# Kernel optimization log

Hardware: AMD Instinct MI355X
Metric: run time of the kernel (lower is better)

The kernel has to match this reference:

```python
import jax, jax.numpy as jnp
import numpy as np

D_MODEL = 1024
N_HEADS = 16
D_K = D_MODEL // N_HEADS
SCALE = 1.0 / np.sqrt(D_K).astype(np.float32)
NEG = -1000000000.0


def setup_inputs() -> dict:
    key = jax.random.key(0)
    ks = jax.random.split(key, 5)
    B, S = 2, 2048
    query = jax.random.normal(ks[0], (B, S, D_MODEL), dtype=jnp.float32)
    k_in = jax.random.normal(ks[1], (B, S, D_MODEL), dtype=jnp.float32)
    v_in = jax.random.normal(ks[2], (B, S, D_MODEL), dtype=jnp.float32)
    # causal mask, broadcast over batch and heads; 0 entries get -1e9
    mask = jnp.tril(jnp.ones((S, S), dtype=jnp.int32))[None, None, :, :]
    w_qkv = jax.random.normal(ks[3], (D_MODEL, 3 * D_MODEL), dtype=jnp.float32) * (1.0 / np.sqrt(D_MODEL))
    w_o = jax.random.normal(ks[4], (D_MODEL, D_MODEL), dtype=jnp.float32) * (1.0 / np.sqrt(D_MODEL))
    return {"query": query, "key": k_in, "value": v_in, "mask": mask, "w_qkv": w_qkv, "w_o": w_o}


def reference(query, key, value, mask, w_qkv, w_o):
    # NOTE: original module ignores `key`/`value`; q,k,v all come from `query`.
    B, S, _ = query.shape
    qkv = query @ w_qkv                       # [B,S,3D]
    q, k, v = jnp.split(qkv, 3, axis=-1)
    def heads(x):
        return x.reshape(B, S, N_HEADS, D_K).transpose(0, 2, 1, 3)  # [B,H,S,dk]
    Q, K, V = heads(q), heads(k), heads(v)
    scores = jnp.einsum('bhqd,bhkd->bhqk', Q, K) * SCALE            # [B,H,S,S]
    scores = jnp.where(mask == 0, NEG, scores)
    attn = jax.nn.softmax(scores, axis=-1)
    # Dropout(0.1) treated as eval-mode identity for a deterministic reference.
    context = jnp.einsum('bhqk,bhkd->bhqd', attn, V)                # [B,H,S,dk]
    context = context.transpose(0, 2, 1, 3).reshape(B, S, D_MODEL)
    return context @ w_o
```

## Files before the change

kernel.cpp:

```cpp
#include <hip/hip_runtime.h>
#include <stdint.h>
#include <type_traits>


typedef __attribute__((ext_vector_type(8))) short bf16x8;
typedef __attribute__((ext_vector_type(4))) float f32x4;

#define LOG2E 1.44269504088896340736f
#define QSCALE (0.125f * LOG2E)

__device__ __forceinline__ unsigned short f2b(float f) {
  union { float f; unsigned int i; } x; x.f = f;
  unsigned int i = x.i;
  return (unsigned short)((i + 0x7FFFu + ((i >> 16) & 1u)) >> 16);
}

__device__ __forceinline__ void async16(const void* g, void* l) {
  __builtin_amdgcn_global_load_lds(
      (__attribute__((address_space(1))) void*)g,
      (__attribute__((address_space(3))) void*)l, 16, 0, 0);
}

__device__ __forceinline__ f32x4 mfma16(bf16x8 a, bf16x8 b, f32x4 c) {
  return __builtin_amdgcn_mfma_f32_16x16x32_bf16(a, b, c, 0, 0, 0);
}

__global__ __launch_bounds__(256) void cvt_x(const float* __restrict__ src,
                                             unsigned short* __restrict__ dst) {
  const size_t i = ((size_t)blockIdx.x * 256 + threadIdx.x) * 8;
  float4 a = *(const float4*)(src + i);
  float4 b = *(const float4*)(src + i + 4);
  unsigned short e[8];
  e[0] = f2b(a.x); e[1] = f2b(a.y); e[2] = f2b(a.z); e[3] = f2b(a.w);
  e[4] = f2b(b.x); e[5] = f2b(b.y); e[6] = f2b(b.z); e[7] = f2b(b.w);
  *(uint4*)(dst + i) = *(const uint4*)e;
}

__global__ __launch_bounds__(256) void transpose_cvt(
    const float* __restrict__ src, unsigned short* __restrict__ dst, int R,
    int Ccols, int scale_cols, float scale) {
  __shared__ __align__(16) unsigned short Lt[64 * 64];
  const int r0 = blockIdx.x * 64, c0 = blockIdx.y * 64;
  const float s = (c0 < scale_cols) ? scale : 1.0f;
  const int t = threadIdx.x;
#pragma unroll
  for (int it = 0; it < 4; ++it) {
    int c = it * 256 + t;
    int sr = c >> 4, co = (c & 15) * 4;
    float4 v = *(const float4*)(src + (size_t)(r0 + sr) * Ccols + c0 + co);
    Lt[(co + 0) * 64 + sr] = f2b(v.x * s);
    Lt[(co + 1) * 64 + sr] = f2b(v.y * s);
    Lt[(co + 2) * 64 + sr] = f2b(v.z * s);
    Lt[(co + 3) * 64 + sr] = f2b(v.w * s);
  }
  __syncthreads();
#pragma unroll
  for (int it = 0; it < 2; ++it) {
    int c = it * 256 + t;
    int dr = c >> 3, so = (c & 7) * 8;
    *(uint4*)(dst + (size_t)(c0 + dr) * R + r0 + so) =
        *(const uint4*)(Lt + dr * 64 + so);
  }
}

template <typename CT>
__global__ __launch_bounds__(256) void gemm_bt(
    const unsigned short* __restrict__ A, const unsigned short* __restrict__ Bt,
    CT* __restrict__ C, int M, int N, int K) {
  __shared__ __align__(16) unsigned short As[128 * 32];
  __shared__ __align__(16) unsigned short Bs[128 * 32];
  const int t = threadIdx.x;
  const int w = t >> 6, l = t & 63;
  const int m0 = blockIdx.y * 128, n0 = blockIdx.x * 128;
  const int wm = (w >> 1) * 64, wn = (w & 1) * 64;
  const int lrow = l & 15, lk = (l >> 4) * 8;

  f32x4 acc[4][4] = {};

  for (int k0 = 0; k0 < K; k0 += 32) {
    __syncthreads();
#pragma unroll
    for (int r = 0; r < 2; ++r) {
      const int c = r * 256 + t;
      async16(A + (size_t)(m0 + (c >> 2)) * K + k0 + (c & 3) * 8,
              As + (size_t)(r * 256 + w * 64) * 8);
      async16(Bt + (size_t)(n0 + (c >> 2)) * K + k0 + (c & 3) * 8,
              Bs + (size_t)(r * 256 + w * 64) * 8);
    }
    asm volatile("s_waitcnt vmcnt(0)" ::: "memory");
    __syncthreads();

    bf16x8 af[4], bf[4];
#pragma unroll
    for (int i = 0; i < 4; ++i)
      af[i] = *(const bf16x8*)(As + (wm + i * 16 + lrow) * 32 + lk);
#pragma unroll
    for (int j = 0; j < 4; ++j)
      bf[j] = *(const bf16x8*)(Bs + (wn + j * 16 + lrow) * 32 + lk);
#pragma unroll
    for (int i = 0; i < 4; ++i)
#pragma unroll
      for (int j = 0; j < 4; ++j)
        acc[i][j] = mfma16(af[i], bf[j], acc[i][j]);
  }

#pragma unroll
  for (int i = 0; i < 4; ++i)
#pragma unroll
    for (int j = 0; j < 4; ++j)
#pragma unroll
      for (int r = 0; r < 4; ++r) {
        int gr = m0 + wm + i * 16 + (l >> 4) * 4 + r;
        int gc = n0 + wn + j * 16 + (l & 15);
        if constexpr (std::is_same<CT, unsigned short>::value)
          C[(size_t)gr * N + gc] = f2b(acc[i][j][r]);
        else
          C[(size_t)gr * N + gc] = acc[i][j][r];
      }
}

__global__ __launch_bounds__(256) void v_relayout(
    const unsigned short* __restrict__ qkv, unsigned short* __restrict__ Vt) {
  __shared__ __align__(16) unsigned short Lt[64 * 64];
  const int s0 = blockIdx.x * 64;
  const int bh = blockIdx.y;
  const int b = bh >> 4, h = bh & 15;
  const int t = threadIdx.x;
#pragma unroll
  for (int r = 0; r < 2; ++r) {
    int c = r * 256 + t;
    int sr = c >> 3, doff = (c & 7) * 8;
    uint4 v = *(const uint4*)(qkv + (size_t)(b * 2048 + s0 + sr) * 3072 + 2048 +
                              h * 64 + doff);
    const unsigned short* e = (const unsigned short*)&v;
#pragma unroll
    for (int j = 0; j < 8; ++j) Lt[(doff + j) * 64 + sr] = e[j];
  }
  __syncthreads();
#pragma unroll
  for (int r = 0; r < 2; ++r) {
    int c = r * 256 + t;
    int dr = c >> 3, so = (c & 7) * 8;
    *(uint4*)(Vt + ((size_t)bh * 64 + dr) * 2048 + s0 + so) =
        *(const uint4*)(Lt + dr * 64 + so);
  }
}

__global__ __launch_bounds__(256) void attn_fwd(
    const unsigned short* __restrict__ qkv,
    const unsigned short* __restrict__ Vt,
    unsigned short* __restrict__ ctx) {
  __shared__ __align__(16) unsigned short Ks[2][64 * 64];
  __shared__ __align__(16) unsigned short Vs[2][64 * 64];
  __shared__ __align__(16) unsigned short Ps[4][16 * 72];

  const int ti = blockIdx.x;
  const int bh = blockIdx.y;
  const int b = bh >> 4, h = bh & 15;
  const int t = threadIdx.x, w = t >> 6, l = t & 63;
  const int lm = l & 15, lq = l >> 4;
  const int sw = lm & 7;
  const int c0 = (lq ^ sw) * 8;
  const int c1 = ((lq + 4) ^ sw) * 8;

  const int qt0[2] = {ti * 64, (31 - ti) * 64};
  const int ktmax = 31 - ti;

  const unsigned short* Qp = qkv + (size_t)(b * 2048) * 3072 + h * 64;
  const unsigned short* Kp = qkv + (size_t)(b * 2048) * 3072 + 1024 + h * 64;
  const unsigned short* Vb = Vt + (size_t)bh * 64 * 2048;

  bf16x8 qf[2][2];
#pragma unroll
  for (int qt = 0; qt < 2; ++qt) {
    const int qrow = qt0[qt] + w * 16 + lm;
    qf[qt][0] = *(const bf16x8*)(Qp + (size_t)qrow * 3072 + lq * 8);
    qf[qt][1] = *(const bf16x8*)(Qp + (size_t)qrow * 3072 + 32 + lq * 8);
  }

  f32x4 oacc[2][4] = {};
  float lsum[2][4] = {{0.f, 0.f, 0.f, 0.f}, {0.f, 0.f, 0.f, 0.f}};

#pragma unroll
  for (int r = 0; r < 2; ++r) {
    int cl = r * 256 + t;
    int row = cl >> 3, cp = cl & 7;
    int so = ((cp ^ (row & 7)) * 8);
    async16(Kp + (size_t)row * 3072 + so,
            Ks[0] + (size_t)(r * 256 + w * 64) * 8);
    async16(Vb + (size_t)row * 2048 + so,
            Vs[0] + (size_t)(r * 256 + w * 64) * 8);
  }

  for (int kt = 0; kt <= ktmax; ++kt) {
    const int cur = kt & 1;
    asm volatile("s_waitcnt vmcnt(0)" ::: "memory");
    __syncthreads();
    if (kt < ktmax) {
      const int nk0 = (kt + 1) * 64;
#pragma unroll
      for (int r = 0; r < 2; ++r) {
        int cl = r * 256 + t;
        int row = cl >> 3, cp = cl & 7;
        int so = ((cp ^ (row & 7)) * 8);
        async16(Kp + (size_t)(nk0 + row) * 3072 + so,
                Ks[cur ^ 1] + (size_t)(r * 256 + w * 64) * 8);
        async16(Vb + (size_t)row * 2048 + nk0 + so,
                Vs[cur ^ 1] + (size_t)(r * 256 + w * 64) * 8);
      }
    }
    const unsigned short* Kc = Ks[cur];
    const unsigned short* Vc = Vs[cur];

#pragma unroll
    for (int qt = 0; qt < 2; ++qt) {
      if (qt == 0 && kt > ti) continue;
      f32x4 sacc[4] = {};
#pragma unroll
      for (int nt = 0; nt < 4; ++nt) {
        const unsigned short* kr = Kc + (nt * 16 + lm) * 64;
        bf16x8 bk0 = *(const bf16x8*)(kr + c0);
        bf16x8 bk1 = *(const bf16x8*)(kr + c1);
        sacc[nt] = mfma16(qf[qt][0], bk0, sacc[nt]);
        sacc[nt] = mfma16(qf[qt][1], bk1, sacc[nt]);
      }

      const bool diag = (kt == ((qt == 0) ? ti : ktmax));
#pragma unroll
      for (int nt = 0; nt < 4; ++nt)
#pragma unroll
        for (int r = 0; r < 4; ++r) {
          float p = exp2f(sacc[nt][r]);
          if (diag && (nt * 16 + lm) > (w * 16 + lq * 4 + r)) p = 0.f;
          lsum[qt][r] += p;
          Ps[w][(lq * 4 + r) * 72 + nt * 16 + lm] = f2b(p);
        }
      asm volatile("s_waitcnt lgkmcnt(0)" ::: "memory");

#pragma unroll
      for (int ks = 0; ks < 2; ++ks) {
        bf16x8 pa = *(const bf16x8*)(&Ps[w][lm * 72 + ks * 32 + lq * 8]);
        const int cc = (ks == 0) ? c0 : c1;
#pragma unroll
        for (int nt = 0; nt < 4; ++nt) {
          bf16x8 vb = *(const bf16x8*)(Vc + (nt * 16 + lm) * 64 + cc);
          oacc[qt][nt] = mfma16(pa, vb, oacc[qt][nt]);
        }
      }
    }
  }

#pragma unroll
  for (int qt = 0; qt < 2; ++qt) {
#pragma unroll
    for (int d = 1; d < 16; d <<= 1)
#pragma unroll
      for (int r = 0; r < 4; ++r)
        lsum[qt][r] += __shfl_xor(lsum[qt][r], d, 64);
    float rinv[4];
#pragma unroll
    for (int r = 0; r < 4; ++r) rinv[r] = 1.f / lsum[qt][r];
#pragma unroll
    for (int nt = 0; nt < 4; ++nt)
#pragma unroll
      for (int r = 0; r < 4; ++r) {
        size_t tok = (size_t)b * 2048 + qt0[qt] + w * 16 + lq * 4 + r;
        ctx[tok * 1024 + h * 64 + nt * 16 + lm] = f2b(oacc[qt][nt][r] * rinv[r]);
      }
  }
}

extern "C" void kernel_launch(void* const* d_in, const int* in_sizes, int n_in,
                              void* d_out, int out_size, void* d_ws,
                              size_t ws_size, hipStream_t stream) {
  const float* query = (const float*)d_in[0];
  const float* w_qkv = (const float*)d_in[4];
  const float* w_o = (const float*)d_in[5];
  float* out = (float*)d_out;

  unsigned short* ws = (unsigned short*)d_ws;
  unsigned short* wqkvT = ws;
  unsigned short* woT = wqkvT + (size_t)3072 * 1024;
  unsigned short* Xb = woT + (size_t)1024 * 1024;
  unsigned short* qkv = Xb + (size_t)4096 * 1024;
  unsigned short* Vt = qkv + (size_t)4096 * 3072;
  unsigned short* ctx = Xb;

  cvt_x<<<dim3(2048), 256, 0, stream>>>(query, Xb);
  transpose_cvt<<<dim3(16, 48), 256, 0, stream>>>(w_qkv, wqkvT, 1024, 3072,
                                                  1024, QSCALE);
  transpose_cvt<<<dim3(16, 16), 256, 0, stream>>>(w_o, woT, 1024, 1024, 0,
                                                  1.0f);
  gemm_bt<unsigned short><<<dim3(24, 32), 256, 0, stream>>>(Xb, wqkvT, qkv,
                                                            4096, 3072, 1024);
  v_relayout<<<dim3(32, 32), 256, 0, stream>>>(qkv, Vt);
  attn_fwd<<<dim3(16, 32), 256, 0, stream>>>(qkv, Vt, ctx);
  gemm_bt<float><<<dim3(8, 32), 256, 0, stream>>>(ctx, woT, out, 4096, 1024,
                                                  1024);
}
```

Before: 232.8 us.

## Split attention KV tiles across two warp groups and shrink output GEMM tile

Attention blocks grow to 512 threads: two groups of four warps each process alternating K/V tiles, then combine partial output accumulators and row sums through shared memory before normalising. This doubles the work in flight per block but drops the double-buffer prefetch overlap and adds a final reduction. The output projection uses a new 64x128-tile GEMM launched on twice as many blocks to fill more CUs. The P-matrix conversion to bf16 now truncates instead of rounding, which saves a few ALU ops at some accuracy cost.

```diff
diff --git a/kernel.cpp b/kernel.cpp
--- a/kernel.cpp
+++ b/kernel.cpp
@@ -13,6 +13,10 @@
   union { float f; unsigned int i; } x; x.f = f;
   unsigned int i = x.i;
   return (unsigned short)((i + 0x7FFFu + ((i >> 16) & 1u)) >> 16);
+}
+__device__ __forceinline__ unsigned short f2b_trunc(float f) {
+  union { float f; unsigned int i; } x; x.f = f;
+  return (unsigned short)(x.i >> 16);
 }
 
 __device__ __forceinline__ void async16(const void* g, void* l) {
@@ -119,6 +123,58 @@
       }
 }
 
+__global__ __launch_bounds__(256) void gemm_o(
+    const unsigned short* __restrict__ A, const unsigned short* __restrict__ Bt,
+    float* __restrict__ C, int M, int N, int K) {
+  __shared__ __align__(16) unsigned short As[64 * 32];
+  __shared__ __align__(16) unsigned short Bs[128 * 32];
+  const int t = threadIdx.x;
+  const int w = t >> 6, l = t & 63;
+  const int m0 = blockIdx.y * 64, n0 = blockIdx.x * 128;
+  const int wm = (w & 1) * 32, wn = (w >> 1) * 64;
+  const int lrow = l & 15, lk = (l >> 4) * 8;
+
+  f32x4 acc[2][4] = {};
+
+  for (int k0 = 0; k0 < K; k0 += 32) {
+    __syncthreads();
+    async16(A + (size_t)(m0 + (t >> 2)) * K + k0 + (t & 3) * 8,
+            As + (size_t)(w * 64) * 8);
+#pragma unroll
+    for (int r = 0; r < 2; ++r) {
+      const int c = r * 256 + t;
+      async16(Bt + (size_t)(n0 + (c >> 2)) * K + k0 + (c & 3) * 8,
+              Bs + (size_t)(r * 256 + w * 64) * 8);
+    }
+    asm volatile("s_waitcnt vmcnt(0)" ::: "memory");
+    __syncthreads();
+
+    bf16x8 af[2], bf[4];
+#pragma unroll
+    for (int i = 0; i < 2; ++i)
+      af[i] = *(const bf16x8*)(As + (wm + i * 16 + lrow) * 32 + lk);
+#pragma unroll
+    for (int j = 0; j < 4; ++j)
+      bf[j] = *(const bf16x8*)(Bs + (wn + j * 16 + lrow) * 32 + lk);
+#pragma unroll
+    for (int i = 0; i < 2; ++i)
+#pragma unroll
+      for (int j = 0; j < 4; ++j)
+        acc[i][j] = mfma16(af[i], bf[j], acc[i][j]);
+  }
+
+#pragma unroll
+  for (int i = 0; i < 2; ++i)
+#pragma unroll
+    for (int j = 0; j < 4; ++j)
+#pragma unroll
+      for (int r = 0; r < 4; ++r) {
+        int gr = m0 + wm + i * 16 + (l >> 4) * 4 + r;
+        int gc = n0 + wn + j * 16 + (l & 15);
+        C[(size_t)gr * N + gc] = acc[i][j][r];
+      }
+}
+
 __global__ __launch_bounds__(256) void v_relayout(
     const unsigned short* __restrict__ qkv, unsigned short* __restrict__ Vt) {
   __shared__ __align__(16) unsigned short Lt[64 * 64];
@@ -146,18 +202,23 @@
   }
 }
 
-__global__ __launch_bounds__(256) void attn_fwd(
+__global__ __launch_bounds__(512) void attn_fwd(
     const unsigned short* __restrict__ qkv,
     const unsigned short* __restrict__ Vt,
     unsigned short* __restrict__ ctx) {
   __shared__ __align__(16) unsigned short Ks[2][64 * 64];
   __shared__ __align__(16) unsigned short Vs[2][64 * 64];
-  __shared__ __align__(16) unsigned short Ps[4][16 * 72];
+  __shared__ __align__(16) unsigned short Ps[8][16 * 72];
 
   const int ti = blockIdx.x;
   const int bh = blockIdx.y;
   const int b = bh >> 4, h = bh & 15;
-  const int t = threadIdx.x, w = t >> 6, l = t & 63;
+  const int t = threadIdx.x;
+  const int g = t >> 8;
+  const int tl = t & 255;
+  const int w = tl >> 6;
+  const int gw = t >> 6;
+  const int l = t & 63;
   const int lm = l & 15, lq = l >> 4;
   const int sw = lm & 7;
   const int c0 = (lq ^ sw) * 8;
@@ -165,6 +226,7 @@
 
   const int qt0[2] = {ti * 64, (31 - ti) * 64};
   const int ktmax = 31 - ti;
+  const int nsup = (ktmax >> 1) + 1;
 
   const unsigned short* Qp = qkv + (size_t)(b * 2048) * 3072 + h * 64;
   const unsigned short* Kp = qkv + (size_t)(b * 2048) * 3072 + 1024 + h * 64;
@@ -181,36 +243,29 @@
   f32x4 oacc[2][4] = {};
   float lsum[2][4] = {{0.f, 0.f, 0.f, 0.f}, {0.f, 0.f, 0.f, 0.f}};
 
-#pragma unroll
-  for (int r = 0; r < 2; ++r) {
-    int cl = r * 256 + t;
-    int row = cl >> 3, cp = cl & 7;
-    int so = ((cp ^ (row & 7)) * 8);
-    async16(Kp + (size_t)row * 3072 + so,
-            Ks[0] + (size_t)(r * 256 + w * 64) * 8);
-    async16(Vb + (size_t)row * 2048 + so,
-            Vs[0] + (size_t)(r * 256 + w * 64) * 8);
-  }
-
-  for (int kt = 0; kt <= ktmax; ++kt) {
-    const int cur = kt & 1;
-    asm volatile("s_waitcnt vmcnt(0)" ::: "memory");
-    __syncthreads();
-    if (kt < ktmax) {
-      const int nk0 = (kt + 1) * 64;
+  for (int jj = 0; jj < nsup; ++jj) {
+    const int kt = 2 * jj + g;
+    const bool have = (kt <= ktmax);
+    __syncthreads();
+    if (have) {
+      const int kk0 = kt * 64;
 #pragma unroll
       for (int r = 0; r < 2; ++r) {
-        int cl = r * 256 + t;
+        int cl = r * 256 + tl;
         int row = cl >> 3, cp = cl & 7;
         int so = ((cp ^ (row & 7)) * 8);
-        async16(Kp + (size_t)(nk0 + row) * 3072 + so,
-                Ks[cur ^ 1] + (size_t)(r * 256 + w * 64) * 8);
-        async16(Vb + (size_t)row * 2048 + nk0 + so,
-                Vs[cur ^ 1] + (size_t)(r * 256 + w * 64) * 8);
-      }
-    }
-    const unsigned short* Kc = Ks[cur];
-    const unsigned short* Vc = Vs[cur];
+        async16(Kp + (size_t)(kk0 + row) * 3072 + so,
+                Ks[g] + (size_t)(r * 256 + w * 64) * 8);
+        async16(Vb + (size_t)row * 2048 + kk0 + so,
+                Vs[g] + (size_t)(r * 256 + w * 64) * 8);
+      }
+    }
+    asm volatile("s_waitcnt vmcnt(0)" ::: "memory");
+    __syncthreads();
+    if (!have) continue;
+
+    const unsigned short* Kc = Ks[g];
+    const unsigned short* Vc = Vs[g];
 
 #pragma unroll
     for (int qt = 0; qt < 2; ++qt) {
@@ -233,13 +288,13 @@
           float p = exp2f(sacc[nt][r]);
           if (diag && (nt * 16 + lm) > (w * 16 + lq * 4 + r)) p = 0.f;
           lsum[qt][r] += p;
-          Ps[w][(lq * 4 + r) * 72 + nt * 16 + lm] = f2b(p);
+          Ps[gw][(lq * 4 + r) * 72 + nt * 16 + lm] = f2b_trunc(p);
         }
       asm volatile("s_waitcnt lgkmcnt(0)" ::: "memory");
 
 #pragma unroll
       for (int ks = 0; ks < 2; ++ks) {
-        bf16x8 pa = *(const bf16x8*)(&Ps[w][lm * 72 + ks * 32 + lq * 8]);
+        bf16x8 pa = *(const bf16x8*)(&Ps[gw][lm * 72 + ks * 32 + lq * 8]);
         const int cc = (ks == 0) ? c0 : c1;
 #pragma unroll
         for (int nt = 0; nt < 4; ++nt) {
@@ -251,22 +306,48 @@
   }
 
 #pragma unroll
-  for (int qt = 0; qt < 2; ++qt) {
+  for (int qt = 0; qt < 2; ++qt)
 #pragma unroll
     for (int d = 1; d < 16; d <<= 1)
 #pragma unroll
       for (int r = 0; r < 4; ++r)
         lsum[qt][r] += __shfl_xor(lsum[qt][r], d, 64);
-    float rinv[4];
-#pragma unroll
-    for (int r = 0; r < 4; ++r) rinv[r] = 1.f / lsum[qt][r];
-#pragma unroll
-    for (int nt = 0; nt < 4; ++nt)
-#pragma unroll
-      for (int r = 0; r < 4; ++r) {
-        size_t tok = (size_t)b * 2048 + qt0[qt] + w * 16 + lq * 4 + r;
-        ctx[tok * 1024 + h * 64 + nt * 16 + lm] = f2b(oacc[qt][nt][r] * rinv[r]);
-      }
+
+  __syncthreads();
+  float* fbuf[2] = {(float*)Ks, (float*)Vs};
+  float* lbuf = (float*)Ps;
+  if (g == 1) {
+#pragma unroll
+    for (int qt = 0; qt < 2; ++qt) {
+#pragma unroll
+      for (int nt = 0; nt < 4; ++nt)
+#pragma unroll
+        for (int r = 0; r < 4; ++r)
+          fbuf[qt][(w * 16 + lq * 4 + r) * 64 + nt * 16 + lm] = oacc[qt][nt][r];
+      if (lm == 0)
+#pragma unroll
+        for (int r = 0; r < 4; ++r)
+          lbuf[qt * 64 + w * 16 + lq * 4 + r] = lsum[qt][r];
+    }
+  }
+  __syncthreads();
+  if (g == 0) {
+#pragma unroll
+    for (int qt = 0; qt < 2; ++qt) {
+      float rinv[4];
+#pragma unroll
+      for (int r = 0; r < 4; ++r)
+        rinv[r] = 1.f / (lsum[qt][r] + lbuf[qt * 64 + w * 16 + lq * 4 + r]);
+#pragma unroll
+      for (int nt = 0; nt < 4; ++nt)
+#pragma unroll
+        for (int r = 0; r < 4; ++r) {
+          float v = oacc[qt][nt][r] +
+                    fbuf[qt][(w * 16 + lq * 4 + r) * 64 + nt * 16 + lm];
+          size_t tok = (size_t)b * 2048 + qt0[qt] + w * 16 + lq * 4 + r;
+          ctx[tok * 1024 + h * 64 + nt * 16 + lm] = f2b(v * rinv[r]);
+        }
+    }
   }
 }
 
@@ -294,7 +375,6 @@
   gemm_bt<unsigned short><<<dim3(24, 32), 256, 0, stream>>>(Xb, wqkvT, qkv,
                                                             4096, 3072, 1024);
   v_relayout<<<dim3(32, 32), 256, 0, stream>>>(qkv, Vt);
-  attn_fwd<<<dim3(16, 32), 256, 0, stream>>>(qkv, Vt, ctx);
-  gemm_bt<float><<<dim3(8, 32), 256, 0, stream>>>(ctx, woT, out, 4096, 1024,
-                                                  1024);
-}
+  attn_fwd<<<dim3(16, 32), 512, 0, stream>>>(qkv, Vt, ctx);
+  gemm_o<<<dim3(8, 64), 256, 0, stream>>>(ctx, woT, out, 4096, 1024, 1024);
+}
```

After: 221.7 us. 1.05x faster.
